# Performance work log

Measured on AMD Instinct MI355X. Metric: run time of the kernel, lower is better.

Reference implementation:

```python
import jax, jax.numpy as jnp
import numpy as np
from jax import lax

VOCAB = 100000; E = 512; HID = 1024; H = HID // 2; T = 7; L = 4096
START = 4; STOP = 5; NEG = -10000.0


def setup_inputs() -> dict:
    key = jax.random.key(0)
    ks = jax.random.split(key, 14)
    s = 0.05  # ~1/sqrt(H), matches torch default init scale
    transitions = jax.random.normal(ks[12], (T, T), dtype=jnp.float32)
    transitions = transitions.at[START, :].set(NEG).at[:, STOP].set(NEG)
    return {
        "sentence": jax.random.randint(ks[0], (L,), 0, VOCAB),
        "emb": jax.random.normal(ks[1], (VOCAB, E), dtype=jnp.float32) * s,
        "w_ih_f": jax.random.normal(ks[2], (4 * H, E), dtype=jnp.float32) * s,
        "w_hh_f": jax.random.normal(ks[3], (4 * H, H), dtype=jnp.float32) * s,
        "b_ih_f": jax.random.normal(ks[4], (4 * H,), dtype=jnp.float32) * s,
        "b_hh_f": jax.random.normal(ks[5], (4 * H,), dtype=jnp.float32) * s,
        "w_ih_b": jax.random.normal(ks[6], (4 * H, E), dtype=jnp.float32) * s,
        "w_hh_b": jax.random.normal(ks[7], (4 * H, H), dtype=jnp.float32) * s,
        "b_ih_b": jax.random.normal(ks[8], (4 * H,), dtype=jnp.float32) * s,
        "b_hh_b": jax.random.normal(ks[9], (4 * H,), dtype=jnp.float32) * s,
        "w_out": jax.random.normal(ks[10], (T, HID), dtype=jnp.float32) * s,
        "b_out": jax.random.normal(ks[11], (T,), dtype=jnp.float32) * s,
        "transitions": transitions,
    }


def _lstm_dir(x, w_ih, w_hh, b_ih, b_hh):
    # x: [L, E] -> hidden states [L, H]; zero initial state (torch default)
    xg = x @ w_ih.T + b_ih  # [L, 4H] precomputed input gates
    h0 = jnp.zeros((H,), x.dtype)
    c0 = jnp.zeros((H,), x.dtype)
    def step(carry, g):
        h, c = carry
        gates = g + w_hh @ h + b_hh
        i, f, gg, o = jnp.split(gates, 4)
        i = jax.nn.sigmoid(i); f = jax.nn.sigmoid(f)
        gg = jnp.tanh(gg); o = jax.nn.sigmoid(o)
        c = f * c + i * gg
        h = o * jnp.tanh(c)
        return (h, c), h
    _, hs = lax.scan(step, (h0, c0), xg)
    return hs


def reference(sentence, emb, w_ih_f, w_hh_f, b_ih_f, b_hh_f,
              w_ih_b, w_hh_b, b_ih_b, b_hh_b, w_out, b_out, transitions):
    x = emb[sentence]  # [L, E]
    hf = _lstm_dir(x, w_ih_f, w_hh_f, b_ih_f, b_hh_f)            # [L, H]
    hb = _lstm_dir(x[::-1], w_ih_b, w_hh_b, b_ih_b, b_hh_b)[::-1]
    feats = jnp.concatenate([hf, hb], axis=1) @ w_out.T + b_out  # [L, T]

    # Viterbi max-plus DP
    init = jnp.full((T,), NEG, feats.dtype).at[START].set(0.0)
    def vstep(fv, feat):
        sc = fv[None, :] + transitions           # [next, prev]
        bp = jnp.argmax(sc, axis=1)
        return jnp.max(sc, axis=1) + feat, bp
    fv, bptrs = lax.scan(vstep, init, feats)     # bptrs: [L, T]
    terminal = fv + transitions[STOP]
    best = jnp.argmax(terminal)
    score = terminal[best]
    # backtrack
    def bt(tag, bp):
        return bp[tag], tag
    _, path_rev = lax.scan(bt, best, bptrs[::-1])
    best_path = path_rev[::-1]                   # [L] tag ids
    return best_path, score
```

## Files before the change

### kernel.cpp

```cpp
#include <hip/hip_runtime.h>
#include <hip/hip_bf16.h>

#define L     4096
#define E     512
#define HID   1024
#define HH    512
#define G4    2048
#define T_TAG 7
#define START_TAG 4
#define STOP_TAG  5
#define NEGV  (-10000.0f)

#define NWRK  32
#define VITB  32
#define NHELP 223
#define NTILE (64 * 2 * 32)
#define SENT  0xFFFFFFFFu

__device__ __forceinline__ unsigned int aload_u(const float* p) {
    return __hip_atomic_load((const unsigned int*)p, __ATOMIC_RELAXED,
                             __HIP_MEMORY_SCOPE_AGENT);
}
__device__ __forceinline__ float aload_f(const float* p) {
    return __uint_as_float(aload_u(p));
}
__device__ __forceinline__ void astore_f(float* p, float x) {
    __hip_atomic_store((unsigned int*)p, __float_as_uint(x),
                       __ATOMIC_RELAXED, __HIP_MEMORY_SCOPE_AGENT);
}

union SMem {
    struct { float h_lds[2][HH]; float glds[8][16]; } wk;
    struct { float As[32][68]; float Bs[32][68]; int sent[64];
             float red[8][8]; } hp;
    struct { unsigned char bp[L][8]; float stage[2][32][8];
             unsigned char gl[64][8]; unsigned char bnd[64]; } vt;
};

__global__ __launch_bounds__(512)
void fused_kernel(const int* __restrict__ sentence, const float* __restrict__ emb,
                  const float* __restrict__ wih_f, const float* __restrict__ bih_f,
                  const float* __restrict__ bhh_f,
                  const float* __restrict__ wih_b, const float* __restrict__ bih_b,
                  const float* __restrict__ bhh_b,
                  const float* __restrict__ whh_f, const float* __restrict__ whh_b,
                  const float* __restrict__ wout, const float* __restrict__ bout,
                  const float* __restrict__ trans,
                  float* __restrict__ xg_f, float* __restrict__ xg_b,
                  float* __restrict__ hf, float* __restrict__ hb,
                  float* __restrict__ feats, float* __restrict__ out, int* cnt)
{
    const int bid = blockIdx.x;
    const int tid = threadIdx.x;

    __shared__ SMem sm;

    if (bid < NWRK) {
        const int dir = bid >> 4;
        const int rnk = bid & 15;

        const float* __restrict__ xg  = dir ? xg_b  : xg_f;
        const float* __restrict__ whh = dir ? whh_b : whh_f;
        float* __restrict__ hout = dir ? hb : hf;

        const int wave = tid >> 6;
        const int lane = tid & 63;
        const int g    = wave >> 1;
        const int jh   = wave & 1;
        const int u0   = rnk * 32;

        float w[16][8];
#pragma unroll
        for (int rr = 0; rr < 16; rr++) {
            const size_t row = (size_t)(g * HH + u0 + jh * 16 + rr);
#pragma unroll
            for (int k = 0; k < 8; k++)
                w[rr][k] = whh[row * HH + (size_t)(k * 64 + lane)];
        }

        float c_state = 0.f;
        const int uu = u0 + (tid & 31);

        auto wait_chunk = [&](int tc) {
            const int* cp = cnt + dir * 64 + tc;
            while (__hip_atomic_load(cp, __ATOMIC_ACQUIRE,
                                     __HIP_MEMORY_SCOPE_AGENT) < 32) {
                __builtin_amdgcn_s_sleep(1);
            }
        };

        float xq0 = 0.f, xq1 = 0.f, xq2 = 0.f, xq3 = 0.f;
        if (tid < 32) {
            wait_chunk(dir ? 63 : 0);
            const float* xgt = xg + (size_t)(dir ? (L - 1) : 0) * G4;
            xq0 = aload_f(xgt + uu);            xq1 = aload_f(xgt + HH + uu);
            xq2 = aload_f(xgt + 2 * HH + uu);   xq3 = aload_f(xgt + 3 * HH + uu);
        }

        for (int s = 0; s < L; s++) {
            const int t = dir ? (L - 1 - s) : s;
            const int p = s & 1;

            unsigned int v = 0;
            if (s > 0) {
                const int tp = dir ? (t + 1) : (t - 1);
                const unsigned int* hp =
                    (const unsigned int*)(hout + (size_t)tp * HH) + tid;
                do {
                    v = __hip_atomic_load(hp, __ATOMIC_RELAXED,
                                          __HIP_MEMORY_SCOPE_AGENT);
                } while (v == SENT);
            }
            sm.wk.h_lds[p][tid] = __uint_as_float(v);
            __syncthreads();

            float hv[8];
#pragma unroll
            for (int k = 0; k < 8; k++) hv[k] = sm.wk.h_lds[p][k * 64 + lane];

            float acc[16];
#pragma unroll
            for (int rr = 0; rr < 16; rr++) {
                float a = 0.f;
#pragma unroll
                for (int k = 0; k < 8; k++) a += w[rr][k] * hv[k];
                acc[rr] = a;
            }

            {
                const bool b0 = lane & 1;
#pragma unroll
                for (int r = 0; r < 8; r++) {
                    const float send = b0 ? acc[r] : acc[r + 8];
                    const float recv = __shfl_xor(send, 1, 64);
                    acc[r] = (b0 ? acc[r + 8] : acc[r]) + recv;
                }
                const bool b1 = lane & 2;
#pragma unroll
                for (int r = 0; r < 4; r++) {
                    const float send = b1 ? acc[r] : acc[r + 4];
                    const float recv = __shfl_xor(send, 2, 64);
                    acc[r] = (b1 ? acc[r + 4] : acc[r]) + recv;
                }
                const bool b2 = lane & 4;
#pragma unroll
                for (int r = 0; r < 2; r++) {
                    const float send = b2 ? acc[r] : acc[r + 2];
                    const float recv = __shfl_xor(send, 4, 64);
                    acc[r] = (b2 ? acc[r + 2] : acc[r]) + recv;
                }
                const bool b3 = lane & 8;
                {
                    const float send = b3 ? acc[0] : acc[1];
                    const float recv = __shfl_xor(send, 8, 64);
                    acc[0] = (b3 ? acc[1] : acc[0]) + recv;
                }
                acc[0] += __shfl_xor(acc[0], 16, 64);
                acc[0] += __shfl_xor(acc[0], 32, 64);
            }
            if (lane < 16) {
                const int R = ((lane & 1) << 3) | ((lane & 2) << 1) |
                              ((lane & 4) >> 1) | ((lane & 8) >> 3);
                sm.wk.glds[wave][R] = acc[0];
            }
            __syncthreads();

            if (tid < 32) {
                const int jh_ = tid >> 4;
                const int rr  = tid & 15;
                float iv = sm.wk.glds[0 + jh_][rr] + xq0;
                float fv = sm.wk.glds[2 + jh_][rr] + xq1;
                float gv = sm.wk.glds[4 + jh_][rr] + xq2;
                float ov = sm.wk.glds[6 + jh_][rr] + xq3;
                iv = 1.f / (1.f + expf(-iv));
                fv = 1.f / (1.f + expf(-fv));
                gv = tanhf(gv);
                ov = 1.f / (1.f + expf(-ov));
                c_state = fv * c_state + iv * gv;
                const float hval = ov * tanhf(c_state);
                __hip_atomic_store((unsigned int*)&hout[(size_t)t * HH + uu],
                                   __float_as_uint(hval), __ATOMIC_RELAXED,
                                   __HIP_MEMORY_SCOPE_AGENT);
                if (s + 1 < L) {
                    const int tn = dir ? (t - 1) : (t + 1);
                    if ((tn & 63) == (dir ? 63 : 0)) wait_chunk(tn >> 6);
                    const float* xgt = xg + (size_t)tn * G4;
                    xq0 = aload_f(xgt + uu);
                    xq1 = aload_f(xgt + HH + uu);
                    xq2 = aload_f(xgt + 2 * HH + uu);
                    xq3 = aload_f(xgt + 3 * HH + uu);
                }
            }
        }
        return;
    }

    if (bid == VITB) {
        if (tid >= 64) return;

        float tr[T_TAG][T_TAG];
#pragma unroll
        for (int i = 0; i < T_TAG; i++)
#pragma unroll
            for (int j = 0; j < T_TAG; j++) tr[i][j] = trans[i * T_TAG + j];

        const int d = tid % T_TAG;
        float trd[T_TAG];
#pragma unroll
        for (int j = 0; j < T_TAG; j++) trd[j] = trans[d * T_TAG + j];
        float trS[T_TAG];
#pragma unroll
        for (int j = 0; j < T_TAG; j++) trS[j] = trans[STOP_TAG * T_TAG + j];

        float fv0 = NEGV, fv1 = NEGV, fv2 = NEGV, fv3 = NEGV,
              fv4 = 0.f,  fv5 = NEGV, fv6 = NEGV;

        bool need[4];
#pragma unroll
        for (int k = 0; k < 4; k++) need[k] = (((tid * 4 + k) & 7) != 7);

        {
            unsigned int v[4] = { SENT, SENT, SENT, SENT };
            int tries = 0;
            for (;;) {
                bool ok = true;
#pragma unroll
                for (int k = 0; k < 4; k++) {
                    const int idx = tid * 4 + k;
                    if (need[k] && v[k] == SENT)
                        v[k] = aload_u(feats + (size_t)(idx >> 3) * 8 + (idx & 7));
                    ok &= (!need[k]) || (v[k] != SENT);
                }
                if (ok) break;
                if (++tries > 2) __builtin_amdgcn_s_sleep(16);
            }
#pragma unroll
            for (int k = 0; k < 4; k++) {
                const int idx = tid * 4 + k;
                sm.vt.stage[0][idx >> 3][idx & 7] =
                    need[k] ? __uint_as_float(v[k]) : 0.f;
            }
        }

        unsigned int pf[4];
#pragma unroll
        for (int k = 0; k < 4; k++) {
            const int idx = tid * 4 + k;
            pf[k] = aload_u(feats + (size_t)(32 + (idx >> 3)) * 8 + (idx & 7));
        }

#define VMAXROW(I, OUT, FI)                                                    \
        {                                                                      \
            const float a0 = fv0 + tr[I][0], a1 = fv1 + tr[I][1];              \
            const float a2 = fv2 + tr[I][2], a3 = fv3 + tr[I][3];              \
            const float a4 = fv4 + tr[I][4], a5 = fv5 + tr[I][5];              \
            const float a6 = fv6 + tr[I][6];                                   \
            const float m012 = fmaxf(fmaxf(a0, a1), a2);                       \
            const float m345 = fmaxf(fmaxf(a3, a4), a5);                       \
            OUT = fmaxf(fmaxf(m012, m345), a6) + (FI);                         \
        }

        for (int b = 0; b < 128; b++) {
            const int cur = b & 1;
            const int t0 = b * 32;
#pragma unroll 8
            for (int q = 0; q < 32; q++) {
                const int T = t0 + q;
                const float4 fa = *(const float4*)&sm.vt.stage[cur][q][0];
                const float4 fb = *(const float4*)&sm.vt.stage[cur][q][4];
                {
                    float bv_ = fv0 + trd[0]; int bj_ = 0; float c_;
                    c_ = fv1 + trd[1]; if (c_ > bv_) { bv_ = c_; bj_ = 1; }
                    c_ = fv2 + trd[2]; if (c_ > bv_) { bv_ = c_; bj_ = 2; }
                    c_ = fv3 + trd[3]; if (c_ > bv_) { bv_ = c_; bj_ = 3; }
                    c_ = fv4 + trd[4]; if (c_ > bv_) { bv_ = c_; bj_ = 4; }
                    c_ = fv5 + trd[5]; if (c_ > bv_) { bv_ = c_; bj_ = 5; }
                    c_ = fv6 + trd[6]; if (c_ > bv_) { bv_ = c_; bj_ = 6; }
                    if (tid < T_TAG) sm.vt.bp[T][tid] = (unsigned char)bj_;
                }
                float nf0, nf1, nf2, nf3, nf4, nf5, nf6;
                VMAXROW(0, nf0, fa.x) VMAXROW(1, nf1, fa.y) VMAXROW(2, nf2, fa.z)
                VMAXROW(3, nf3, fa.w) VMAXROW(4, nf4, fb.x) VMAXROW(5, nf5, fb.y)
                VMAXROW(6, nf6, fb.z)
                fv0 = nf0; fv1 = nf1; fv2 = nf2; fv3 = nf3;
                fv4 = nf4; fv5 = nf5; fv6 = nf6;
            }
            if (b + 1 < 128) {
#pragma unroll
                for (int k = 0; k < 4; k++) {
                    const int idx = tid * 4 + k;
                    if (need[k]) {
                        while (pf[k] == SENT)
                            pf[k] = aload_u(feats +
                                    (size_t)((b + 1) * 32 + (idx >> 3)) * 8 + (idx & 7));
                        sm.vt.stage[cur ^ 1][idx >> 3][idx & 7] = __uint_as_float(pf[k]);
                    } else {
                        sm.vt.stage[cur ^ 1][idx >> 3][idx & 7] = 0.f;
                    }
                }
                if (b + 2 < 128) {
#pragma unroll
                    for (int k = 0; k < 4; k++) {
                        const int idx = tid * 4 + k;
                        pf[k] = aload_u(feats +
                                (size_t)((b + 2) * 32 + (idx >> 3)) * 8 + (idx & 7));
                    }
                }
            }
        }
#undef VMAXROW

        int bt_final; float best_score;
        {
            float bv_ = fv0 + trS[0]; int bj_ = 0; float c_;
            c_ = fv1 + trS[1]; if (c_ > bv_) { bv_ = c_; bj_ = 1; }
            c_ = fv2 + trS[2]; if (c_ > bv_) { bv_ = c_; bj_ = 2; }
            c_ = fv3 + trS[3]; if (c_ > bv_) { bv_ = c_; bj_ = 3; }
            c_ = fv4 + trS[4]; if (c_ > bv_) { bv_ = c_; bj_ = 4; }
            c_ = fv5 + trS[5]; if (c_ > bv_) { bv_ = c_; bj_ = 5; }
            c_ = fv6 + trS[6]; if (c_ > bv_) { bv_ = c_; bj_ = 6; }
            bt_final = bj_; best_score = bv_;
        }

        const int lo = 64 * tid + 1;
        const int hi = (tid == 63) ? (L - 1) : (64 * tid + 64);
        {
            unsigned int c0 = 0, c1 = 1, c2 = 2, c3 = 3, c4 = 4, c5 = 5, c6 = 6;
            for (int t = hi; t >= lo; --t) {
                const unsigned char* row = &sm.vt.bp[t][0];
                c0 = row[c0]; c1 = row[c1]; c2 = row[c2]; c3 = row[c3];
                c4 = row[c4]; c5 = row[c5]; c6 = row[c6];
            }
            sm.vt.gl[tid][0] = (unsigned char)c0; sm.vt.gl[tid][1] = (unsigned char)c1;
            sm.vt.gl[tid][2] = (unsigned char)c2; sm.vt.gl[tid][3] = (unsigned char)c3;
            sm.vt.gl[tid][4] = (unsigned char)c4; sm.vt.gl[tid][5] = (unsigned char)c5;
            sm.vt.gl[tid][6] = (unsigned char)c6;
        }
        if (tid == 0) {
            int b = bt_final;
            for (int l2 = 63; l2 >= 0; --l2) {
                sm.vt.bnd[l2] = (unsigned char)b;
                b = sm.vt.gl[l2][b];
            }
        }
        {
            int tag = sm.vt.bnd[tid];
            for (int t = hi; t >= lo; --t) {
                tag = sm.vt.bp[t][tag];
                out[t - 1] = (float)tag;
            }
        }
        if (tid == 63) {
            out[L - 1] = (float)bt_final;
            out[L]     = best_score;
        }
        return;
    }

    const int hid_ = bid - (NWRK + 1);

    for (int tile = hid_; tile < NTILE; tile += NHELP) {
        const int jt = tile & 31;
        const int sd = tile >> 5;
        const int dr = sd & 1;
        const int sc = sd >> 1;
        const int t0 = dr ? (L - 64 - sc * 64) : (sc * 64);
        const int j0 = jt * 64;
        const float* __restrict__ wih = dr ? wih_b : wih_f;
        const float* __restrict__ bih = dr ? bih_b : bih_f;
        const float* __restrict__ bhh = dr ? bhh_b : bhh_f;
        float* __restrict__ xg = dr ? xg_b : xg_f;

        if (tid < 64) sm.hp.sent[tid] = sentence[t0 + tid];

        const int li = tid >> 3;
        const int k4 = (tid & 7) * 4;
        const int tx = tid & 15;
        const int ty = tid >> 4;

        float a00 = 0.f, a01 = 0.f, a02 = 0.f, a03 = 0.f;
        float a10 = 0.f, a11 = 0.f, a12 = 0.f, a13 = 0.f;

        for (int k0 = 0; k0 < E; k0 += 32) {
            __syncthreads();
            {
                const float4 av = *(const float4*)(emb + (size_t)sm.hp.sent[li] * E + k0 + k4);
                sm.hp.As[k4 + 0][li] = av.x; sm.hp.As[k4 + 1][li] = av.y;
                sm.hp.As[k4 + 2][li] = av.z; sm.hp.As[k4 + 3][li] = av.w;
                const float4 bv = *(const float4*)(wih + (size_t)(j0 + li) * E + k0 + k4);
                sm.hp.Bs[k4 + 0][li] = bv.x; sm.hp.Bs[k4 + 1][li] = bv.y;
                sm.hp.Bs[k4 + 2][li] = bv.z; sm.hp.Bs[k4 + 3][li] = bv.w;
            }
            __syncthreads();
#pragma unroll
            for (int k = 0; k < 32; k++) {
                const float a0 = sm.hp.As[k][ty * 2 + 0];
                const float a1 = sm.hp.As[k][ty * 2 + 1];
                const float4 b4 = *(const float4*)&sm.hp.Bs[k][tx * 4];
                a00 += a0 * b4.x; a01 += a0 * b4.y; a02 += a0 * b4.z; a03 += a0 * b4.w;
                a10 += a1 * b4.x; a11 += a1 * b4.y; a12 += a1 * b4.z; a13 += a1 * b4.w;
            }
        }

        {
            const int c0 = j0 + tx * 4;
            const float bsum0 = bih[c0 + 0] + bhh[c0 + 0];
            const float bsum1 = bih[c0 + 1] + bhh[c0 + 1];
            const float bsum2 = bih[c0 + 2] + bhh[c0 + 2];
            const float bsum3 = bih[c0 + 3] + bhh[c0 + 3];
            float* r0 = xg + (size_t)(t0 + ty * 2 + 0) * G4 + c0;
            float* r1 = xg + (size_t)(t0 + ty * 2 + 1) * G4 + c0;
            astore_f(r0 + 0, a00 + bsum0); astore_f(r0 + 1, a01 + bsum1);
            astore_f(r0 + 2, a02 + bsum2); astore_f(r0 + 3, a03 + bsum3);
            astore_f(r1 + 0, a10 + bsum0); astore_f(r1 + 1, a11 + bsum1);
            astore_f(r1 + 2, a12 + bsum2); astore_f(r1 + 3, a13 + bsum3);
        }
        __syncthreads();
        if (tid == 0)
            __hip_atomic_fetch_add(&cnt[dr * 64 + (t0 >> 6)], 1,
                                   __ATOMIC_RELEASE, __HIP_MEMORY_SCOPE_AGENT);
    }

    const int wave = tid >> 6, lane = tid & 63;
    for (int t = hid_; t < L; t += NHELP) {
        if (tid < 32) {
            const float* src = (tid < 16) ? hf : hb;
            const unsigned int* wp =
                (const unsigned int*)(src + (size_t)t * HH) + (tid & 15) * 32;
            while (__hip_atomic_load(wp, __ATOMIC_RELAXED,
                                     __HIP_MEMORY_SCOPE_AGENT) == SENT) {
                __builtin_amdgcn_s_sleep(8);
            }
        }
        __syncthreads();

        const unsigned int* p0 = (const unsigned int*)(hf + (size_t)t * HH) + tid;
        const unsigned int* p1 = (const unsigned int*)(hb + (size_t)t * HH) + tid;
        unsigned int v0, v1;
        do { v0 = __hip_atomic_load(p0, __ATOMIC_RELAXED,
                                    __HIP_MEMORY_SCOPE_AGENT); } while (v0 == SENT);
        do { v1 = __hip_atomic_load(p1, __ATOMIC_RELAXED,
                                    __HIP_MEMORY_SCOPE_AGENT); } while (v1 == SENT);
        const float x0 = __uint_as_float(v0);
        const float x1 = __uint_as_float(v1);

        float acc[T_TAG];
#pragma unroll
        for (int i = 0; i < T_TAG; i++)
            acc[i] = x0 * wout[i * HID + tid] + x1 * wout[i * HID + HH + tid];
#pragma unroll
        for (int m = 1; m < 64; m <<= 1) {
#pragma unroll
            for (int i = 0; i < T_TAG; i++) acc[i] += __shfl_xor(acc[i], m, 64);
        }
        if (lane == 0) {
#pragma unroll
            for (int i = 0; i < T_TAG; i++) sm.hp.red[wave][i] = acc[i];
        }
        __syncthreads();
        if (tid < 8) {
            float ssum = 0.f;
            if (tid < T_TAG) {
                ssum = bout[tid];
#pragma unroll
                for (int wv = 0; wv < 8; wv++) ssum += sm.hp.red[wv][tid];
            }
            astore_f(&feats[(size_t)t * 8 + tid], ssum);
        }
        __syncthreads();
    }
}

extern "C" void kernel_launch(void* const* d_in, const int* in_sizes, int n_in,
                              void* d_out, int out_size, void* d_ws, size_t ws_size,
                              hipStream_t stream)
{
    const int*   sentence = (const int*)  d_in[0];
    const float* emb      = (const float*)d_in[1];
    const float* wih_f    = (const float*)d_in[2];
    const float* whh_f    = (const float*)d_in[3];
    const float* bih_f    = (const float*)d_in[4];
    const float* bhh_f    = (const float*)d_in[5];
    const float* wih_b    = (const float*)d_in[6];
    const float* whh_b    = (const float*)d_in[7];
    const float* bih_b    = (const float*)d_in[8];
    const float* bhh_b    = (const float*)d_in[9];
    const float* wout     = (const float*)d_in[10];
    const float* bout     = (const float*)d_in[11];
    const float* trans    = (const float*)d_in[12];
    float* out = (float*)d_out;

    char* ws = (char*)d_ws;
    int*   cnt    = (int*)ws;
    float* xg_f   = (float*)(ws + 1024);
    float* xg_b   = xg_f  + (size_t)L * G4;
    float* hfbuf  = xg_b  + (size_t)L * G4;
    float* hbbuf  = hfbuf + (size_t)L * HH;
    float* featsb = hbbuf + (size_t)L * HH;

    hipMemsetAsync(cnt, 0, 1024, stream);
    hipMemsetAsync(hfbuf, 0xFF,
                   ((size_t)2 * L * HH + (size_t)L * 8) * sizeof(float), stream);

    void* args[] = { (void*)&sentence, (void*)&emb,
                     (void*)&wih_f, (void*)&bih_f, (void*)&bhh_f,
                     (void*)&wih_b, (void*)&bih_b, (void*)&bhh_b,
                     (void*)&whh_f, (void*)&whh_b,
                     (void*)&wout, (void*)&bout, (void*)&trans,
                     (void*)&xg_f, (void*)&xg_b,
                     (void*)&hfbuf, (void*)&hbbuf,
                     (void*)&featsb, (void*)&out, (void*)&cnt };
    hipLaunchCooperativeKernel((void*)fused_kernel, dim3(256),
                               dim3(512), args, 0, stream);
}
```

Before: 8.724 ms.

## Parallelize Viterbi forward pass via chunked max-plus matrix products

Replaces the sequential 4096-step Viterbi recurrence in one wave with a chunked max-plus scan. Each of 64 lanes composes a 7x7 max-plus transfer matrix over its 64-step chunk, one lane chains the 64 chunk matrices to get each chunk's entry vector, and every lane then replays its own chunk to record backpointers. This shortens the serial dependency chain from 4096 steps to roughly three passes of 64, at the cost of about 7x more arithmetic per step and heavy register use for the matrices. It also drops the LDS double-buffered feature staging. Each lane now spin-waits on its own chunk's features, which the LSTM blocks may produce late, so chunks near the end of the sequence may stall.

```diff
diff --git a/kernel.cpp b/kernel.cpp
--- a/kernel.cpp
+++ b/kernel.cpp
@@ -33,7 +33,10 @@
     struct { float h_lds[2][HH]; float glds[8][16]; } wk;
     struct { float As[32][68]; float Bs[32][68]; int sent[64];
              float red[8][8]; } hp;
-    struct { unsigned char bp[L][8]; float stage[2][32][8];
+    struct { unsigned char bp[L][8];
+             float gm[64][T_TAG][T_TAG];
+             float ebuf[64][T_TAG];
+             float fin_score; int fin_tag;
              unsigned char gl[64][8]; unsigned char bnd[64]; } vt;
 };
 
@@ -203,115 +206,117 @@
         for (int i = 0; i < T_TAG; i++)
 #pragma unroll
             for (int j = 0; j < T_TAG; j++) tr[i][j] = trans[i * T_TAG + j];
-
-        const int d = tid % T_TAG;
-        float trd[T_TAG];
-#pragma unroll
-        for (int j = 0; j < T_TAG; j++) trd[j] = trans[d * T_TAG + j];
         float trS[T_TAG];
 #pragma unroll
         for (int j = 0; j < T_TAG; j++) trS[j] = trans[STOP_TAG * T_TAG + j];
 
-        float fv0 = NEGV, fv1 = NEGV, fv2 = NEGV, fv3 = NEGV,
-              fv4 = 0.f,  fv5 = NEGV, fv6 = NEGV;
-
-        bool need[4];
-#pragma unroll
-        for (int k = 0; k < 4; k++) need[k] = (((tid * 4 + k) & 7) != 7);
-
+        const int t0 = tid * 64;
+
+        float M[T_TAG][T_TAG];
+        float f[T_TAG];
         {
-            unsigned int v[4] = { SENT, SENT, SENT, SENT };
-            int tries = 0;
-            for (;;) {
-                bool ok = true;
-#pragma unroll
-                for (int k = 0; k < 4; k++) {
-                    const int idx = tid * 4 + k;
-                    if (need[k] && v[k] == SENT)
-                        v[k] = aload_u(feats + (size_t)(idx >> 3) * 8 + (idx & 7));
-                    ok &= (!need[k]) || (v[k] != SENT);
-                }
-                if (ok) break;
-                if (++tries > 2) __builtin_amdgcn_s_sleep(16);
-            }
-#pragma unroll
-            for (int k = 0; k < 4; k++) {
-                const int idx = tid * 4 + k;
-                sm.vt.stage[0][idx >> 3][idx & 7] =
-                    need[k] ? __uint_as_float(v[k]) : 0.f;
-            }
-        }
-
-        unsigned int pf[4];
-#pragma unroll
-        for (int k = 0; k < 4; k++) {
-            const int idx = tid * 4 + k;
-            pf[k] = aload_u(feats + (size_t)(32 + (idx >> 3)) * 8 + (idx & 7));
-        }
-
-#define VMAXROW(I, OUT, FI)                                                    \
+#pragma unroll
+            for (int i = 0; i < T_TAG; i++) {
+                unsigned int v;
+                const float* p = feats + (size_t)t0 * 8 + i;
+                do { v = aload_u(p); } while (v == SENT);
+                f[i] = __uint_as_float(v);
+            }
+#pragma unroll
+            for (int i = 0; i < T_TAG; i++)
+#pragma unroll
+                for (int j = 0; j < T_TAG; j++) M[i][j] = tr[i][j] + f[i];
+        }
+        for (int q = 1; q < 64; q++) {
+            const int T = t0 + q;
+#pragma unroll
+            for (int i = 0; i < T_TAG; i++) {
+                unsigned int v;
+                const float* p = feats + (size_t)T * 8 + i;
+                do { v = aload_u(p); } while (v == SENT);
+                f[i] = __uint_as_float(v);
+            }
+#pragma unroll
+            for (int j = 0; j < T_TAG; j++) {
+                float c[T_TAG];
+#pragma unroll
+                for (int k = 0; k < T_TAG; k++) c[k] = M[k][j];
+#pragma unroll
+                for (int i = 0; i < T_TAG; i++) {
+                    float m = tr[i][0] + c[0];
+#pragma unroll
+                    for (int k = 1; k < T_TAG; k++)
+                        m = fmaxf(m, tr[i][k] + c[k]);
+                    M[i][j] = f[i] + m;
+                }
+            }
+        }
+
+#pragma unroll
+        for (int i = 0; i < T_TAG; i++)
+#pragma unroll
+            for (int j = 0; j < T_TAG; j++) sm.vt.gm[tid][i][j] = M[i][j];
+        asm volatile("s_waitcnt lgkmcnt(0)" ::: "memory");
+
+        if (tid == 0) {
+            float e[T_TAG];
+#pragma unroll
+            for (int i = 0; i < T_TAG; i++)
+                e[i] = (i == START_TAG) ? 0.f : NEGV;
+#pragma unroll
+            for (int i = 0; i < T_TAG; i++) sm.vt.ebuf[0][i] = e[i];
+            for (int l = 0; l < 63; l++) {
+                float en[T_TAG];
+#pragma unroll
+                for (int i = 0; i < T_TAG; i++) {
+                    float m = sm.vt.gm[l][i][0] + e[0];
+#pragma unroll
+                    for (int k = 1; k < T_TAG; k++)
+                        m = fmaxf(m, sm.vt.gm[l][i][k] + e[k]);
+                    en[i] = m;
+                }
+#pragma unroll
+                for (int i = 0; i < T_TAG; i++) {
+                    e[i] = en[i];
+                    sm.vt.ebuf[l + 1][i] = e[i];
+                }
+            }
+        }
+        asm volatile("s_waitcnt lgkmcnt(0)" ::: "memory");
+
+        float fv0 = sm.vt.ebuf[tid][0], fv1 = sm.vt.ebuf[tid][1],
+              fv2 = sm.vt.ebuf[tid][2], fv3 = sm.vt.ebuf[tid][3],
+              fv4 = sm.vt.ebuf[tid][4], fv5 = sm.vt.ebuf[tid][5],
+              fv6 = sm.vt.ebuf[tid][6];
+
+#define ADEST(I, T, NF)                                                        \
         {                                                                      \
-            const float a0 = fv0 + tr[I][0], a1 = fv1 + tr[I][1];              \
-            const float a2 = fv2 + tr[I][2], a3 = fv3 + tr[I][3];              \
-            const float a4 = fv4 + tr[I][4], a5 = fv5 + tr[I][5];              \
-            const float a6 = fv6 + tr[I][6];                                   \
-            const float m012 = fmaxf(fmaxf(a0, a1), a2);                       \
-            const float m345 = fmaxf(fmaxf(a3, a4), a5);                       \
-            OUT = fmaxf(fmaxf(m012, m345), a6) + (FI);                         \
-        }
-
-        for (int b = 0; b < 128; b++) {
-            const int cur = b & 1;
-            const int t0 = b * 32;
-#pragma unroll 8
-            for (int q = 0; q < 32; q++) {
-                const int T = t0 + q;
-                const float4 fa = *(const float4*)&sm.vt.stage[cur][q][0];
-                const float4 fb = *(const float4*)&sm.vt.stage[cur][q][4];
-                {
-                    float bv_ = fv0 + trd[0]; int bj_ = 0; float c_;
-                    c_ = fv1 + trd[1]; if (c_ > bv_) { bv_ = c_; bj_ = 1; }
-                    c_ = fv2 + trd[2]; if (c_ > bv_) { bv_ = c_; bj_ = 2; }
-                    c_ = fv3 + trd[3]; if (c_ > bv_) { bv_ = c_; bj_ = 3; }
-                    c_ = fv4 + trd[4]; if (c_ > bv_) { bv_ = c_; bj_ = 4; }
-                    c_ = fv5 + trd[5]; if (c_ > bv_) { bv_ = c_; bj_ = 5; }
-                    c_ = fv6 + trd[6]; if (c_ > bv_) { bv_ = c_; bj_ = 6; }
-                    if (tid < T_TAG) sm.vt.bp[T][tid] = (unsigned char)bj_;
-                }
-                float nf0, nf1, nf2, nf3, nf4, nf5, nf6;
-                VMAXROW(0, nf0, fa.x) VMAXROW(1, nf1, fa.y) VMAXROW(2, nf2, fa.z)
-                VMAXROW(3, nf3, fa.w) VMAXROW(4, nf4, fb.x) VMAXROW(5, nf5, fb.y)
-                VMAXROW(6, nf6, fb.z)
-                fv0 = nf0; fv1 = nf1; fv2 = nf2; fv3 = nf3;
-                fv4 = nf4; fv5 = nf5; fv6 = nf6;
-            }
-            if (b + 1 < 128) {
-#pragma unroll
-                for (int k = 0; k < 4; k++) {
-                    const int idx = tid * 4 + k;
-                    if (need[k]) {
-                        while (pf[k] == SENT)
-                            pf[k] = aload_u(feats +
-                                    (size_t)((b + 1) * 32 + (idx >> 3)) * 8 + (idx & 7));
-                        sm.vt.stage[cur ^ 1][idx >> 3][idx & 7] = __uint_as_float(pf[k]);
-                    } else {
-                        sm.vt.stage[cur ^ 1][idx >> 3][idx & 7] = 0.f;
-                    }
-                }
-                if (b + 2 < 128) {
-#pragma unroll
-                    for (int k = 0; k < 4; k++) {
-                        const int idx = tid * 4 + k;
-                        pf[k] = aload_u(feats +
-                                (size_t)((b + 2) * 32 + (idx >> 3)) * 8 + (idx & 7));
-                    }
-                }
-            }
-        }
-#undef VMAXROW
-
-        int bt_final; float best_score;
-        {
+            float bv_ = fv0 + tr[I][0]; int bj_ = 0; float c_;                 \
+            c_ = fv1 + tr[I][1]; if (c_ > bv_) { bv_ = c_; bj_ = 1; }          \
+            c_ = fv2 + tr[I][2]; if (c_ > bv_) { bv_ = c_; bj_ = 2; }          \
+            c_ = fv3 + tr[I][3]; if (c_ > bv_) { bv_ = c_; bj_ = 3; }          \
+            c_ = fv4 + tr[I][4]; if (c_ > bv_) { bv_ = c_; bj_ = 4; }          \
+            c_ = fv5 + tr[I][5]; if (c_ > bv_) { bv_ = c_; bj_ = 5; }          \
+            c_ = fv6 + tr[I][6]; if (c_ > bv_) { bv_ = c_; bj_ = 6; }          \
+            sm.vt.bp[(T)][I] = (unsigned char)bj_;                             \
+            NF = bv_ + f[I];                                                   \
+        }
+
+        for (int q = 0; q < 64; q++) {
+            const int T = t0 + q;
+#pragma unroll
+            for (int i = 0; i < T_TAG; i++)
+                f[i] = aload_f(feats + (size_t)T * 8 + i);
+            float nf0, nf1, nf2, nf3, nf4, nf5, nf6;
+            ADEST(0, T, nf0) ADEST(1, T, nf1) ADEST(2, T, nf2)
+            ADEST(3, T, nf3) ADEST(4, T, nf4) ADEST(5, T, nf5)
+            ADEST(6, T, nf6)
+            fv0 = nf0; fv1 = nf1; fv2 = nf2; fv3 = nf3;
+            fv4 = nf4; fv5 = nf5; fv6 = nf6;
+        }
+#undef ADEST
+
+        if (tid == 63) {
             float bv_ = fv0 + trS[0]; int bj_ = 0; float c_;
             c_ = fv1 + trS[1]; if (c_ > bv_) { bv_ = c_; bj_ = 1; }
             c_ = fv2 + trS[2]; if (c_ > bv_) { bv_ = c_; bj_ = 2; }
@@ -319,8 +324,12 @@
             c_ = fv4 + trS[4]; if (c_ > bv_) { bv_ = c_; bj_ = 4; }
             c_ = fv5 + trS[5]; if (c_ > bv_) { bv_ = c_; bj_ = 5; }
             c_ = fv6 + trS[6]; if (c_ > bv_) { bv_ = c_; bj_ = 6; }
-            bt_final = bj_; best_score = bv_;
-        }
+            sm.vt.fin_tag = bj_;
+            sm.vt.fin_score = bv_;
+        }
+        asm volatile("s_waitcnt lgkmcnt(0)" ::: "memory");
+        const int bt_final = sm.vt.fin_tag;
+        const float best_score = sm.vt.fin_score;
 
         const int lo = 64 * tid + 1;
         const int hi = (tid == 63) ? (L - 1) : (64 * tid + 64);
@@ -336,6 +345,7 @@
             sm.vt.gl[tid][4] = (unsigned char)c4; sm.vt.gl[tid][5] = (unsigned char)c5;
             sm.vt.gl[tid][6] = (unsigned char)c6;
         }
+        asm volatile("s_waitcnt lgkmcnt(0)" ::: "memory");
         if (tid == 0) {
             int b = bt_final;
             for (int l2 = 63; l2 >= 0; --l2) {
@@ -343,6 +353,7 @@
                 b = sm.vt.gl[l2][b];
             }
         }
+        asm volatile("s_waitcnt lgkmcnt(0)" ::: "memory");
         {
             int tag = sm.vt.bnd[tid];
             for (int t = hi; t >= lo; --t) {
```

Result: faster. 8.012 ms (-8.2%).
